# Optimization experiments

Hardware: AMD Instinct MI355X
Metric: run time of the kernel (lower is better)

The kernel has to match this reference:

```python
import jax, jax.numpy as jnp
import numpy as np

INPUT_DIM = 1024
OUTPUT_DIM = 1024
DEGREE = 8


def pentanacci_basis(x, degree):
    # x: [B, I] (already sigmoided). Returns [B, I, degree+1].
    # P0 = 0, P1 = 1, P2 = x, P3 = x, P4 = x^2,
    # Pn = x*P(n-1) + P(n-2) + P(n-3) + P(n-4) + P(n-5) for n >= 5
    zeros = jnp.zeros_like(x)
    ones = jnp.ones_like(x)
    seeds = [zeros, ones, x, x, x * x]
    basis = seeds[: degree + 1]
    for n in range(5, degree + 1):
        basis.append(x * basis[n - 1] + basis[n - 2] + basis[n - 3]
                     + basis[n - 4] + basis[n - 5])
    return jnp.stack(basis, axis=-1)


def setup_inputs() -> dict:
    key = jax.random.key(0)
    kx, kw = jax.random.split(key)
    x = jax.random.normal(kx, (4096, INPUT_DIM), dtype=jnp.float32)
    std = 1.0 / (INPUT_DIM * (DEGREE + 1))
    coeffs = std * jax.random.normal(kw, (INPUT_DIM, OUTPUT_DIM, DEGREE + 1),
                                     dtype=jnp.float32)
    return {"x": x, "coeffs": coeffs}


def reference(x, coeffs):
    degree = coeffs.shape[-1] - 1
    xs = jax.nn.sigmoid(x)                      # [B, I]
    basis = pentanacci_basis(xs, degree)        # [B, I, D+1]
    y = jnp.einsum('bid,iod->bo', basis, coeffs)  # [B, O]
    return y
```

## Files before the change

### kernel.cpp

```cpp
#include <hip/hip_runtime.h>
#include <stdint.h>

#define M_DIM 4096
#define I_DIM 1024
#define O_DIM 1024
#define KB 6
#define K_DIM (I_DIM * KB)
#define SPLITS 4

typedef __attribute__((ext_vector_type(8))) short short8;
typedef __attribute__((ext_vector_type(4))) float f32x4;
typedef __attribute__((ext_vector_type(4))) unsigned int u32x4;
typedef __attribute__((ext_vector_type(4))) float hfloat4;
typedef __attribute__((ext_vector_type(8))) _Float16 h16x8;

__device__ __forceinline__ unsigned short f2bf(float f) {
  union { float f; unsigned int u; } v; v.f = f;
  unsigned int u = v.u;
  unsigned int r = (u + 0x7FFFu + ((u >> 16) & 1u)) >> 16;
  return (unsigned short)r;
}

__global__ __launch_bounds__(256) void k_prep(const float* __restrict__ x,
                                              const float* __restrict__ C,
                                              unsigned short* __restrict__ A,
                                              unsigned short* __restrict__ Bt,
                                              float* __restrict__ partB) {
  const int bid = blockIdx.x;
  if (bid < 2048) {
    int t = bid * 256 + threadIdx.x;
    long e0 = (long)t * 8;
    const hfloat4* xp = (const hfloat4*)(x + e0);
    hfloat4 v0 = xp[0], v1 = xp[1];
    float xv[8];
    xv[0]=v0[0]; xv[1]=v0[1]; xv[2]=v0[2]; xv[3]=v0[3];
    xv[4]=v1[0]; xv[5]=v1[1]; xv[6]=v1[2]; xv[7]=v1[3];
    unsigned short outv[48];
#pragma unroll
    for (int e = 0; e < 8; ++e) {
      float s  = 1.0f / (1.0f + __expf(-xv[e]));
      float b2 = s, b3 = s, b4 = s * s;
      float b5 = fmaf(s, b4, b3 + b2 + 1.0f);
      float b6 = fmaf(s, b5, b4 + b3 + b2 + 1.0f);
      float b7 = fmaf(s, b6, b5 + b4 + b3 + b2);
      float b8 = fmaf(s, b7, b6 + b5 + b4 + b3);
      outv[e*6+0] = f2bf(s);
      outv[e*6+1] = f2bf(b4);
      outv[e*6+2] = f2bf(b5);
      outv[e*6+3] = f2bf(b6);
      outv[e*6+4] = f2bf(b7);
      outv[e*6+5] = f2bf(b8);
    }
    u32x4* dst = (u32x4*)(A + e0 * KB);
    const u32x4* srcv = (const u32x4*)outv;
#pragma unroll
    for (int q = 0; q < 6; ++q) dst[q] = srcv[q];
  } else {
    __shared__ unsigned short tile[32 * 192];
    __shared__ float bred[256];
    int b = bid - 2048;
    int i0 = (b & 31) * 32, o0 = (b >> 5) * 32;
    int t = threadIdx.x;
    int ol = t & 31, ig = t >> 5;
    float bsum = 0.f;
#pragma unroll
    for (int r = 0; r < 4; ++r) {
      int il = ig + r * 8;
      const float* p = C + (size_t)(i0 + il) * (O_DIM * 9) + (size_t)(o0 + ol) * 9;
      float c1 = p[1];
      float c2 = p[2], c3 = p[3], c4 = p[4], c5 = p[5], c6 = p[6], c7 = p[7], c8 = p[8];
      bsum += c1;
      unsigned short* q = &tile[ol * 192 + il * 6];
      q[0] = f2bf(c2 + c3);
      q[1] = f2bf(c4);
      q[2] = f2bf(c5);
      q[3] = f2bf(c6);
      q[4] = f2bf(c7);
      q[5] = f2bf(c8);
    }
    bred[t] = bsum;
    __syncthreads();
    if (t < 32) {
      float s = 0.f;
#pragma unroll
      for (int g = 0; g < 8; ++g) s += bred[g * 32 + t];
      partB[(size_t)(b & 31) * O_DIM + o0 + t] = s;
    }
    const u32x4* lsrc = (const u32x4*)tile;
#pragma unroll
    for (int r = 0; r < 3; ++r) {
      int c = t + r * 256;
      int row = c / 24, off = c % 24;
      u32x4* gdst = (u32x4*)(Bt + (size_t)(o0 + row) * K_DIM + (size_t)i0 * 6 + off * 8);
      *gdst = lsrc[c];
    }
  }
}

__global__ __launch_bounds__(256) void k_bias2(const float* __restrict__ partB,
                                               float* __restrict__ bias) {
  int o = blockIdx.x * 256 + threadIdx.x;
  float s = 0.f;
#pragma unroll
  for (int ib = 0; ib < 32; ++ib) s += partB[(size_t)ib * O_DIM + o];
  bias[o] = s;
}

#define SBAR __builtin_amdgcn_sched_barrier(0)

template<bool SPLIT>
__global__ __launch_bounds__(512, 2) void k_gemm8(const unsigned short* __restrict__ A,
                                                  const unsigned short* __restrict__ B,
                                                  const float* __restrict__ bias,
                                                  void* __restrict__ dst) {
  constexpr int CK = SPLIT ? (K_DIM / SPLITS) : K_DIM;
  constexpr int NT = CK / 64;
  constexpr int PPX = SPLIT ? 8 : 2;
  __shared__ char lds[131072];
  const int tid = threadIdx.x;
  const int lane = tid & 63, wid = tid >> 6;
  const int wm = wid >> 2, wn = wid & 3;
  const int l15 = lane & 15, lk = lane >> 4, l7 = lane & 7;
  const int flat = blockIdx.x + (blockIdx.y << 2) + (blockIdx.z << 6);
  const int xcd = flat & 7, slot = flat >> 3;
  const int panel = xcd * PPX + (slot >> 2);
  const int xn = slot & 3;
  const int ym = panel & 15, zk = panel >> 4;
  const int m0 = ym * 256, n0 = xn * 256;
  const size_t kb = (size_t)zk * CK;
  const int srow = tid >> 3;
  const int cg8 = (((tid & 7) ^ ((tid >> 3) & 7)) * 8);
  const int cx0 = (lk ^ l7) * 16;
  const int cx1 = ((4 + lk) ^ l7) * 16;
  const int arow = wm * 128 + l15;
  const int brow = wn * 64 + l15;

  auto gload = [&](const unsigned short* s, int ldsoff) {
    __builtin_amdgcn_global_load_lds((const __attribute__((address_space(1))) void*)s,
        (__attribute__((address_space(3))) void*)(lds + ldsoff), 16, 0, 0);
  };
  auto stageA = [&](int buf, int h, int kt2) {
    const unsigned short* s = A + (size_t)(m0 + h * 128 + srow) * K_DIM + kb + (size_t)kt2 * 64 + cg8;
    int d = buf * 65536 + h * 16384 + tid * 16;
    gload(s, d);
    gload(s + (size_t)64 * K_DIM, d + 8192);
  };
  auto stageB = [&](int buf, int h, int kt2) {
    const unsigned short* s = B + (size_t)(n0 + h * 128 + srow) * K_DIM + kb + (size_t)kt2 * 64 + cg8;
    int d = buf * 65536 + 32768 + h * 16384 + tid * 16;
    gload(s, d);
    gload(s + (size_t)64 * K_DIM, d + 8192);
  };

  short8 af0[4][2], af1[4][2], bf0[2][2], bf1[2][2];
  f32x4 acc[8][4];
#pragma unroll
  for (int i = 0; i < 8; ++i)
#pragma unroll
    for (int n = 0; n < 4; ++n)
#pragma unroll
      for (int j = 0; j < 4; ++j) acc[i][n][j] = 0.f;

  auto loadA = [&](int buf, int h, short8 (&afx)[4][2]) {
#pragma unroll
    for (int mm = 0; mm < 4; ++mm) {
      int rb = buf * 65536 + (arow + h * 64 + mm * 16) * 128;
      afx[mm][0] = *(const short8*)(lds + rb + cx0);
      afx[mm][1] = *(const short8*)(lds + rb + cx1);
    }
  };
  auto loadB = [&](int buf, int g, short8 (&bfx)[2][2]) {
#pragma unroll
    for (int nn = 0; nn < 2; ++nn) {
      int rb = buf * 65536 + 32768 + (brow + g * 32 + nn * 16) * 128;
      bfx[nn][0] = *(const short8*)(lds + rb + cx0);
      bfx[nn][1] = *(const short8*)(lds + rb + cx1);
    }
  };
  auto quad = [&](short8 (&afx)[4][2], int h, int g, short8 (&bfx)[2][2]) {
#pragma unroll
    for (int mm = 0; mm < 4; ++mm)
#pragma unroll
      for (int nn = 0; nn < 2; ++nn)
#pragma unroll
        for (int kc = 0; kc < 2; ++kc)
          acc[h * 4 + mm][g * 2 + nn] =
              __builtin_amdgcn_mfma_f32_16x16x32_bf16(afx[mm][kc], bfx[nn][kc],
                                                      acc[h * 4 + mm][g * 2 + nn], 0, 0, 0);
  };

  stageA(0, 0, 0); stageA(0, 1, 0); stageB(0, 0, 0); stageB(0, 1, 0);
  asm volatile("s_waitcnt vmcnt(0)" ::: "memory"); SBAR;
  __builtin_amdgcn_s_barrier(); SBAR;

#pragma unroll 1
  for (int kt = 0; kt < NT; ++kt) {
    const int buf = kt & 1, nb = buf ^ 1;
    if (kt + 1 < NT) {
      stageA(nb, 0, kt + 1); stageA(nb, 1, kt + 1);
      stageB(nb, 0, kt + 1); stageB(nb, 1, kt + 1);
    }
    loadA(buf, 0, af0); loadB(buf, 0, bf0);
    loadB(buf, 1, bf1); loadA(buf, 1, af1);
    __builtin_amdgcn_s_setprio(1);
    quad(af0, 0, 0, bf0); quad(af0, 0, 1, bf1);
    quad(af1, 1, 1, bf1); quad(af1, 1, 0, bf0);
    __builtin_amdgcn_s_setprio(0); SBAR;
    if (kt + 1 < NT) {
      asm volatile("s_waitcnt vmcnt(0)" ::: "memory"); SBAR;
      __builtin_amdgcn_s_barrier(); SBAR;
    }
  }

  if (SPLIT) {
    _Float16* base = (_Float16*)dst + (size_t)zk * ((size_t)M_DIM * O_DIM);
#pragma unroll
    for (int mi = 0; mi < 8; ++mi) {
      int r0 = m0 + wm * 128 + mi * 16 + (lk << 2);
#pragma unroll
      for (int ni = 0; ni < 4; ++ni) {
        int col = n0 + wn * 64 + ni * 16 + l15;
#pragma unroll
        for (int j = 0; j < 4; ++j)
          base[(size_t)(r0 + j) * O_DIM + col] = (_Float16)acc[mi][ni][j];
      }
    }
  } else {
    float* base = (float*)dst;
#pragma unroll
    for (int mi = 0; mi < 8; ++mi) {
      int r0 = m0 + wm * 128 + mi * 16 + (lk << 2);
#pragma unroll
      for (int ni = 0; ni < 4; ++ni) {
        int col = n0 + wn * 64 + ni * 16 + l15;
        float bv = bias[col];
#pragma unroll
        for (int j = 0; j < 4; ++j)
          base[(size_t)(r0 + j) * O_DIM + col] = acc[mi][ni][j] + bv;
      }
    }
  }
}

__global__ __launch_bounds__(256) void k_reduce(const _Float16* __restrict__ part,
                                                const float* __restrict__ bias,
                                                float* __restrict__ out) {
  size_t t = (size_t)blockIdx.x * 256 + threadIdx.x;
  size_t idx = t * 8;
  const size_t P = (size_t)M_DIM * O_DIM;
  h16x8 s0 = *(const h16x8*)(part + idx);
  h16x8 s1 = *(const h16x8*)(part + P + idx);
  h16x8 s2 = *(const h16x8*)(part + 2 * P + idx);
  h16x8 s3 = *(const h16x8*)(part + 3 * P + idx);
  size_t bo = idx & (O_DIM - 1);
  f32x4 b0 = *(const f32x4*)(bias + bo);
  f32x4 b1 = *(const f32x4*)(bias + bo + 4);
  f32x4 r0, r1;
#pragma unroll
  for (int j = 0; j < 4; ++j) {
    r0[j] = (((float)s0[j] + (float)s1[j]) + ((float)s2[j] + (float)s3[j])) + b0[j];
    r1[j] = (((float)s0[j+4] + (float)s1[j+4]) + ((float)s2[j+4] + (float)s3[j+4])) + b1[j];
  }
  *(f32x4*)(out + idx) = r0;
  *(f32x4*)(out + idx + 4) = r1;
}

extern "C" void kernel_launch(void* const* d_in, const int* in_sizes, int n_in,
                              void* d_out, int out_size, void* d_ws, size_t ws_size,
                              hipStream_t stream) {
  const float* x      = (const float*)d_in[0];
  const float* coeffs = (const float*)d_in[1];
  float* out = (float*)d_out;
  char* ws = (char*)d_ws;
  const size_t offA     = 0;
  const size_t offB     = 50331648;
  const size_t offBias  = offB + 12582912;
  const size_t offPartB = offBias + 4096;
  const size_t offPart  = offPartB + 131072;
  const size_t needSplit = offPart + (size_t)SPLITS * M_DIM * O_DIM * 2;

  unsigned short* A  = (unsigned short*)(ws + offA);
  unsigned short* Bt = (unsigned short*)(ws + offB);
  float* bias        = (float*)(ws + offBias);
  float* partB       = (float*)(ws + offPartB);
  _Float16* part     = (_Float16*)(ws + offPart);

  k_prep<<<3072, 256, 0, stream>>>(x, coeffs, A, Bt, partB);
  k_bias2<<<4, 256, 0, stream>>>(partB, bias);

  if (ws_size >= needSplit) {
    k_gemm8<true><<<dim3(O_DIM / 256, M_DIM / 256, SPLITS), 512, 0, stream>>>(A, Bt, bias, (void*)part);
    k_reduce<<<(M_DIM * O_DIM) / (256 * 8), 256, 0, stream>>>(part, bias, out);
  } else {
    k_gemm8<false><<<dim3(O_DIM / 256, M_DIM / 256, 1), 512, 0, stream>>>(A, Bt, bias, (void*)out);
  }
}
```

Baseline: 88.23 us.

## Split K-tile into two halves and prefetch next tile's LDS fragments across barrier

```diff
diff --git a/kernel.cpp b/kernel.cpp
--- a/kernel.cpp
+++ b/kernel.cpp
@@ -152,7 +152,7 @@
     gload(s + (size_t)64 * K_DIM, d + 8192);
   };
 
-  short8 af0[4][2], af1[4][2], bf0[2][2], bf1[2][2];
+  short8 a0[8], b0v[4], a1[8], b1v[4];
   f32x4 acc[8][4];
 #pragma unroll
   for (int i = 0; i < 8; ++i)
@@ -161,37 +161,26 @@
 #pragma unroll
       for (int j = 0; j < 4; ++j) acc[i][n][j] = 0.f;
 
-  auto loadA = [&](int buf, int h, short8 (&afx)[4][2]) {
-#pragma unroll
-    for (int mm = 0; mm < 4; ++mm) {
-      int rb = buf * 65536 + (arow + h * 64 + mm * 16) * 128;
-      afx[mm][0] = *(const short8*)(lds + rb + cx0);
-      afx[mm][1] = *(const short8*)(lds + rb + cx1);
-    }
-  };
-  auto loadB = [&](int buf, int g, short8 (&bfx)[2][2]) {
-#pragma unroll
-    for (int nn = 0; nn < 2; ++nn) {
-      int rb = buf * 65536 + 32768 + (brow + g * 32 + nn * 16) * 128;
-      bfx[nn][0] = *(const short8*)(lds + rb + cx0);
-      bfx[nn][1] = *(const short8*)(lds + rb + cx1);
-    }
-  };
-  auto quad = [&](short8 (&afx)[4][2], int h, int g, short8 (&bfx)[2][2]) {
-#pragma unroll
-    for (int mm = 0; mm < 4; ++mm)
-#pragma unroll
-      for (int nn = 0; nn < 2; ++nn)
-#pragma unroll
-        for (int kc = 0; kc < 2; ++kc)
-          acc[h * 4 + mm][g * 2 + nn] =
-              __builtin_amdgcn_mfma_f32_16x16x32_bf16(afx[mm][kc], bfx[nn][kc],
-                                                      acc[h * 4 + mm][g * 2 + nn], 0, 0, 0);
+  auto readK = [&](int buf, int cx, short8 (&av)[8], short8 (&bv)[4]) {
+#pragma unroll
+    for (int mi = 0; mi < 8; ++mi)
+      av[mi] = *(const short8*)(lds + buf * 65536 + (arow + mi * 16) * 128 + cx);
+#pragma unroll
+    for (int ni = 0; ni < 4; ++ni)
+      bv[ni] = *(const short8*)(lds + buf * 65536 + 32768 + (brow + ni * 16) * 128 + cx);
+  };
+  auto quadK = [&](short8 (&av)[8], short8 (&bv)[4]) {
+#pragma unroll
+    for (int mi = 0; mi < 8; ++mi)
+#pragma unroll
+      for (int ni = 0; ni < 4; ++ni)
+        acc[mi][ni] = __builtin_amdgcn_mfma_f32_16x16x32_bf16(av[mi], bv[ni], acc[mi][ni], 0, 0, 0);
   };
 
   stageA(0, 0, 0); stageA(0, 1, 0); stageB(0, 0, 0); stageB(0, 1, 0);
   asm volatile("s_waitcnt vmcnt(0)" ::: "memory"); SBAR;
   __builtin_amdgcn_s_barrier(); SBAR;
+  readK(0, cx0, a0, b0v);
 
 #pragma unroll 1
   for (int kt = 0; kt < NT; ++kt) {
@@ -200,16 +189,19 @@
       stageA(nb, 0, kt + 1); stageA(nb, 1, kt + 1);
       stageB(nb, 0, kt + 1); stageB(nb, 1, kt + 1);
     }
-    loadA(buf, 0, af0); loadB(buf, 0, bf0);
-    loadB(buf, 1, bf1); loadA(buf, 1, af1);
+    readK(buf, cx1, a1, b1v);
     __builtin_amdgcn_s_setprio(1);
-    quad(af0, 0, 0, bf0); quad(af0, 0, 1, bf1);
-    quad(af1, 1, 1, bf1); quad(af1, 1, 0, bf0);
+    quadK(a0, b0v);
     __builtin_amdgcn_s_setprio(0); SBAR;
+    asm volatile("s_waitcnt lgkmcnt(0)" ::: "memory"); SBAR;
     if (kt + 1 < NT) {
       asm volatile("s_waitcnt vmcnt(0)" ::: "memory"); SBAR;
       __builtin_amdgcn_s_barrier(); SBAR;
-    }
+      readK(nb, cx0, a0, b0v);
+    }
+    __builtin_amdgcn_s_setprio(1);
+    quadK(a1, b1v);
+    __builtin_amdgcn_s_setprio(0); SBAR;
   }
 
   if (SPLIT) {
```

Result: no change. 86.94 us (-1.5%).
